# Performance work log

Hardware: AMD Instinct MI355X
Metric: run time of the kernel (lower is better)

Reference implementation:

```python
import jax, jax.numpy as jnp
import numpy as np

N_NODES = 19000   # STRING PPI nodes
N_EDGES = 600000  # avg degree ~32
B = 4096          # batch of perturbations
GNN = 256         # gnn_dim
H = 512           # hidden_dim
MID = 2048        # hidden_dim * expand
L = 6             # n_layers residual blocks
C = 3             # n_classes
R = 512           # bilinear_rank
G = 6640          # n_genes_out
LN_EPS = 1e-5


def _ln(x, scale, bias):
    mu = jnp.mean(x, axis=-1, keepdims=True)
    var = jnp.var(x, axis=-1, keepdims=True)
    return (x - mu) * jax.lax.rsqrt(var + LN_EPS) * scale + bias


def setup_inputs() -> dict:
    key = jax.random.key(0)
    ks = iter(jax.random.split(key, 24))
    s = lambda *sh: jax.random.normal(next(ks), sh, dtype=jnp.float32) * 0.02
    inp = {
        # -1 marks unknown genes (fallback embedding path)
        "node_indices": jax.random.randint(next(ks), (B,), -1, N_NODES),
        "edge_index": jax.random.randint(next(ks), (2, N_EDGES), 0, N_NODES),
        "edge_weight": jax.random.uniform(next(ks), (N_EDGES,), dtype=jnp.float32),
        # frozen mps.0-6 output cache (detached buffer in torch)
        "node_emb_cache": jax.random.normal(next(ks), (N_NODES, GNN), dtype=jnp.float32),
        # trainable graph tail (mps.7 modeled as GraphConv) + post_mp Linear
        "w_root": s(GNN, GNN),
        "w_neigh": s(GNN, GNN),
        "w_post": s(GNN, GNN),
        "b_post": jnp.zeros((GNN,), jnp.float32),
        "fallback_emb": s(GNN),
        # input_proj: LayerNorm(256) + Linear(256->512, no bias)
        "ln_in_scale": jnp.ones((GNN,), jnp.float32),
        "ln_in_bias": jnp.zeros((GNN,), jnp.float32),
        "w_in": s(H, GNN),
        # 6 residual blocks, stacked params
        "rb_ln_scale": jnp.ones((L, H), jnp.float32),
        "rb_ln_bias": jnp.zeros((L, H), jnp.float32),
        "rb_fc1": s(L, MID, H),
        "rb_fc2": s(L, H, MID),
        # bilinear head
        "w_bilinear": s(C * R, H),
        "out_gene_emb": s(G, R),
    }
    return inp


def reference(node_indices, edge_index, edge_weight, node_emb_cache,
              w_root, w_neigh, w_post, b_post, fallback_emb,
              ln_in_scale, ln_in_bias, w_in,
              rb_ln_scale, rb_ln_bias, rb_fc1, rb_fc2,
              w_bilinear, out_gene_emb):
    # --- trainable graph tail: mps.7 (GraphConv) + post_mp ---
    src, dst = edge_index[0], edge_index[1]
    msg = node_emb_cache[src] * edge_weight[:, None]          # [E, GNN]
    agg = jax.ops.segment_sum(msg, dst, num_segments=N_NODES)  # [N, GNN]
    x = jax.nn.relu(node_emb_cache @ w_root.T + agg @ w_neigh.T)
    node_emb = x @ w_post.T + b_post                           # [N, GNN]

    # --- gather perturbation embeddings with fallback for -1 ---
    known = node_indices >= 0
    safe = jnp.clip(node_indices, 0, None)
    pert = jnp.where(known[:, None], node_emb[safe], fallback_emb[None, :])  # [B, GNN]

    # --- input_proj + 6 residual blocks (dropout inactive in eval) ---
    h = _ln(pert, ln_in_scale, ln_in_bias) @ w_in.T            # [B, H]
    for i in range(L):
        y = _ln(h, rb_ln_scale[i], rb_ln_bias[i])
        y = jax.nn.gelu(y @ rb_fc1[i].T, approximate=False)    # exact erf GELU (torch default)
        h = y @ rb_fc2[i].T + h

    # --- bilinear head ---
    blin = (h @ w_bilinear.T).reshape(-1, C, R)                # [B, 3, R]
    logits = jnp.einsum('bcr,gr->bcg', blin, out_gene_emb)     # [B, 3, G]
    return logits
```

## Files before the change

### kernel.cpp

```cpp
#include <hip/hip_runtime.h>
#include <hip/hip_bf16.h>

#define N_NODES 19000
#define N_EDGES 600000
#define BATCH   4096
#define GNN_D   256
#define H_D     512
#define MID_D   2048
#define L_N     6
#define C_N     3
#define R_D     512
#define G_N     6640
#define LN_EPS  1e-5f
#define MAXDEG  128

typedef __attribute__((ext_vector_type(8))) short short8;
typedef __attribute__((ext_vector_type(4))) float f32x4;
typedef __hip_bfloat16 bf16;


__global__ void f32_to_bf16_kernel(const float* __restrict__ in, bf16* __restrict__ out, int n4) {
  int i = blockIdx.x * blockDim.x + threadIdx.x;
  if (i >= n4) return;
  float4 v = ((const float4*)in)[i];
  out[i * 4 + 0] = __float2bfloat16(v.x);
  out[i * 4 + 1] = __float2bfloat16(v.y);
  out[i * 4 + 2] = __float2bfloat16(v.z);
  out[i * 4 + 3] = __float2bfloat16(v.w);
}

__global__ void build_wrn_kernel(const float* __restrict__ w_root,
                                 const float* __restrict__ w_neigh,
                                 bf16* __restrict__ out) {
  int i4 = blockIdx.x * blockDim.x + threadIdx.x;
  if (i4 >= GNN_D * 2 * GNN_D / 4) return;
  int base = i4 * 4;
  int n = base >> 9;
  int k = base & 511;
  const float* src = (k < GNN_D) ? (w_root + (size_t)n * GNN_D + k)
                                 : (w_neigh + (size_t)n * GNN_D + (k - GNN_D));
  float4 v = *(const float4*)src;
  out[base + 0] = __float2bfloat16(v.x);
  out[base + 1] = __float2bfloat16(v.y);
  out[base + 2] = __float2bfloat16(v.z);
  out[base + 3] = __float2bfloat16(v.w);
}

__global__ void init_meta_kernel(int* __restrict__ flags, int* __restrict__ cursor,
                                 int* __restrict__ nuniq) {
  int i = blockIdx.x * blockDim.x + threadIdx.x;
  if (i < N_NODES) flags[i] = 0;
  if (i < BATCH) cursor[i] = 0;
  if (i == 0) *nuniq = 0;
}

__global__ void mark_needed_kernel(const int* __restrict__ idx, int* __restrict__ flags) {
  int i = blockIdx.x * blockDim.x + threadIdx.x;
  if (i < BATCH) {
    int id = idx[i];
    if (id >= 0) flags[id] = 1;
  }
}

__global__ void assign_slots_kernel(const int* __restrict__ flags, int* __restrict__ slot,
                                    int* __restrict__ uniq, int* __restrict__ nuniq) {
  int i = blockIdx.x * blockDim.x + threadIdx.x;
  if (i >= N_NODES) return;
  if (flags[i]) {
    int s = atomicAdd(nuniq, 1);
    slot[i] = s;
    uniq[s] = i;
  }
}

__global__ __launch_bounds__(256) void fill_edges_kernel(
    const int* __restrict__ ei, const float* __restrict__ ew,
    const int* __restrict__ flags, const int* __restrict__ slot,
    int* __restrict__ cursor, int* __restrict__ el_src, float* __restrict__ el_w) {
  int e = blockIdx.x * blockDim.x + threadIdx.x;
  if (e >= N_EDGES) return;
  int dst = ei[N_EDGES + e];
  if (!flags[dst]) return;
  int s = slot[dst];
  int p = atomicAdd(&cursor[s], 1);
  if (p < MAXDEG) {
    el_src[s * MAXDEG + p] = ei[e];
    el_w[s * MAXDEG + p] = ew[e];
  }
}

__global__ __launch_bounds__(256) void gather_nodes_kernel(
    const float* __restrict__ cache, const int* __restrict__ uniq,
    const int* __restrict__ cursor, const int* __restrict__ nuniq,
    const int* __restrict__ el_src, const float* __restrict__ el_w,
    bf16* __restrict__ compact2) {
  int s = blockIdx.x, t = threadIdx.x;
  bf16* row = compact2 + (size_t)s * (2 * GNN_D);
  if (s >= *nuniq) {
    row[t] = __float2bfloat16(0.f);
    row[GNN_D + t] = __float2bfloat16(0.f);
    return;
  }
  row[t] = __float2bfloat16(cache[(size_t)uniq[s] * GNN_D + t]);
  int deg = cursor[s];
  deg = (deg < MAXDEG) ? deg : MAXDEG;
  float acc = 0.f;
  for (int e = 0; e < deg; ++e) {
    int src = el_src[s * MAXDEG + e];
    float w = el_w[s * MAXDEG + e];
    acc += cache[(size_t)src * GNN_D + t] * w;
  }
  row[GNN_D + t] = __float2bfloat16(acc);
}

__global__ __launch_bounds__(256) void gather_ln_kernel(
    const float* __restrict__ embc, const int* __restrict__ slot,
    const float* __restrict__ fallback, const int* __restrict__ idx,
    const float* __restrict__ scale, const float* __restrict__ bias,
    bf16* __restrict__ out) {
  int b = blockIdx.x, t = threadIdx.x;
  int id = idx[b];
  float v = (id >= 0) ? embc[(size_t)slot[id] * GNN_D + t] : fallback[t];
  float s = v, q = v * v;
#pragma unroll
  for (int o = 32; o > 0; o >>= 1) { s += __shfl_down(s, o); q += __shfl_down(q, o); }
  __shared__ float ls[4], lq[4];
  int wv = t >> 6, ln = t & 63;
  if (ln == 0) { ls[wv] = s; lq[wv] = q; }
  __syncthreads();
  s = ls[0] + ls[1] + ls[2] + ls[3];
  q = lq[0] + lq[1] + lq[2] + lq[3];
  float mu = s * (1.f / GNN_D);
  float var = q * (1.f / GNN_D) - mu * mu;
  float r = rsqrtf(var + LN_EPS);
  out[(size_t)b * GNN_D + t] = __float2bfloat16((v - mu) * r * scale[t] + bias[t]);
}

__global__ __launch_bounds__(256) void ln512_kernel(
    const float* __restrict__ x, const float* __restrict__ scale,
    const float* __restrict__ bias, bf16* __restrict__ out) {
  int b = blockIdx.x, t = threadIdx.x;
  const float* xr = x + (size_t)b * H_D;
  float v0 = xr[t];
  float v1 = xr[256 + t];
  float s = v0 + v1, q = v0 * v0 + v1 * v1;
#pragma unroll
  for (int o = 32; o > 0; o >>= 1) { s += __shfl_down(s, o); q += __shfl_down(q, o); }
  __shared__ float ls[4], lq[4];
  int wv = t >> 6, ln = t & 63;
  if (ln == 0) { ls[wv] = s; lq[wv] = q; }
  __syncthreads();
  s = ls[0] + ls[1] + ls[2] + ls[3];
  q = lq[0] + lq[1] + lq[2] + lq[3];
  float mu = s * (1.f / H_D);
  float var = q * (1.f / H_D) - mu * mu;
  float r = rsqrtf(var + LN_EPS);
  bf16* orow = out + (size_t)b * H_D;
  orow[t]       = __float2bfloat16((v0 - mu) * r * scale[t]       + bias[t]);
  orow[256 + t] = __float2bfloat16((v1 - mu) * r * scale[256 + t] + bias[256 + t]);
}

__device__ inline float gelu_exact(float x) {
  return 0.5f * x * (1.f + erff(x * 0.70710678118654752f));
}


template <int NBN, int ACT, int OUT_BF16, int ADDC, int BIAS, int HBF, int SWZ>
__global__ __launch_bounds__(256) void gemm_mfma_kernel(
    const bf16* __restrict__ A, const bf16* __restrict__ W,
    const float* __restrict__ bias, const float* __restrict__ addC,
    void* __restrict__ Cout, bf16* __restrict__ out2,
    int M, int N, int K, int gx) {
  constexpr int BN = NBN * 64;
  constexpr int NF_N = NBN * 2;
  __shared__ __align__(16) bf16 sA[128 * 32];
  __shared__ __align__(16) bf16 sB[BN * 32];
  const int tid = threadIdx.x;
  const int lane = tid & 63;
  const int wid = tid >> 6;
  const int wr = wid >> 1, wc = wid & 1;

  int bidx, bidy;
  if (SWZ) {
    int nwg = gridDim.x;
    int bid = blockIdx.x;
    int q = nwg >> 3, r = nwg & 7;
    int xcd = bid & 7, orig = bid >> 3;
    int swz = (xcd < r ? xcd * (q + 1) : r * (q + 1) + (xcd - r) * q) + orig;
    bidx = swz % gx;
    bidy = swz / gx;
  } else {
    bidx = blockIdx.x;
    bidy = blockIdx.y;
  }
  const int bm = bidx * 128, bn = bidy * BN;

  f32x4 acc[4][NF_N];
#pragma unroll
  for (int m = 0; m < 4; ++m)
#pragma unroll
    for (int n = 0; n < NF_N; ++n) acc[m][n] = (f32x4){0.f, 0.f, 0.f, 0.f};

  const int rbase = lane & 15;
  const int g = lane >> 4;

  for (int k0 = 0; k0 < K; k0 += 32) {
#pragma unroll
    for (int i = 0; i < 2; ++i) {
      int li = i * 256 + tid;
      int row = li >> 2;
      int kq = (li & 3) << 3;
      int ar = bm + row; ar = (ar < M) ? ar : (M - 1);
      __builtin_amdgcn_global_load_lds(
          (const __attribute__((address_space(1))) void*)(A + (size_t)ar * K + k0 + kq),
          (__attribute__((address_space(3))) void*)(sA + li * 8), 16, 0, 0);
    }
#pragma unroll
    for (int i = 0; i < NBN; ++i) {
      int li = i * 256 + tid;
      int row = li >> 2;
      int kq = (li & 3) << 3;
      int br = bn + row; br = (br < N) ? br : (N - 1);
      __builtin_amdgcn_global_load_lds(
          (const __attribute__((address_space(1))) void*)(W + (size_t)br * K + k0 + kq),
          (__attribute__((address_space(3))) void*)(sB + li * 8), 16, 0, 0);
    }
    __syncthreads();

    short8 af[4], bfrag[NF_N];
#pragma unroll
    for (int m = 0; m < 4; ++m)
      af[m] = *(const short8*)(sA + (wr * 64 + m * 16 + rbase) * 32 + g * 8);
#pragma unroll
    for (int n = 0; n < NF_N; ++n)
      bfrag[n] = *(const short8*)(sB + (wc * (NBN * 32) + n * 16 + rbase) * 32 + g * 8);
#pragma unroll
    for (int m = 0; m < 4; ++m)
#pragma unroll
      for (int n = 0; n < NF_N; ++n)
        acc[m][n] = __builtin_amdgcn_mfma_f32_16x16x32_bf16(af[m], bfrag[n], acc[m][n], 0, 0, 0);
    __syncthreads();
  }

  const int rb = (lane >> 4) * 4;
  const int cb = lane & 15;
#pragma unroll
  for (int m = 0; m < 4; ++m) {
#pragma unroll
    for (int n = 0; n < NF_N; ++n) {
      int col = bn + wc * (NBN * 32) + n * 16 + cb;
      if (col >= N) continue;
      int row0 = bm + wr * 64 + m * 16 + rb;
#pragma unroll
      for (int r = 0; r < 4; ++r) {
        int row = row0 + r;
        if (row >= M) continue;
        float v = acc[m][n][r];
        if (BIAS) v += bias[col];
        if (ADDC) v += addC[(size_t)row * N + col];
        if (ACT == 1) v = fmaxf(v, 0.f);
        if (ACT == 2) v = gelu_exact(v);
        if (OUT_BF16)
          ((bf16*)Cout)[(size_t)row * N + col] = __float2bfloat16(v);
        else
          ((float*)Cout)[(size_t)row * N + col] = v;
        if (HBF)
          out2[(size_t)row * N + col] = __float2bfloat16(v);
      }
    }
  }
}

template <int NBN, int ACT, int OUT_BF16, int ADDC, int BIAS, int HBF>
static void launch_mfma(const bf16* A, const bf16* W, const float* bias,
                        const float* addC, void* C, bf16* out2,
                        int M, int N, int K, hipStream_t stream) {
  dim3 grid(M / 128, (N + NBN * 64 - 1) / (NBN * 64));
  gemm_mfma_kernel<NBN, ACT, OUT_BF16, ADDC, BIAS, HBF, 0>
      <<<grid, 256, 0, stream>>>(A, W, bias, addC, C, out2, M, N, K, 0);
}


#define MB (1024u * 1024u)

extern "C" void kernel_launch(void* const* d_in, const int* in_sizes, int n_in,
                              void* d_out, int out_size, void* d_ws, size_t ws_size,
                              hipStream_t stream) {
  const int*   node_indices = (const int*)d_in[0];
  const int*   edge_index   = (const int*)d_in[1];
  const float* edge_weight  = (const float*)d_in[2];
  const float* cache        = (const float*)d_in[3];
  const float* w_root       = (const float*)d_in[4];
  const float* w_neigh      = (const float*)d_in[5];
  const float* w_post       = (const float*)d_in[6];
  const float* b_post       = (const float*)d_in[7];
  const float* fallback     = (const float*)d_in[8];
  const float* ln_in_scale  = (const float*)d_in[9];
  const float* ln_in_bias   = (const float*)d_in[10];
  const float* w_in         = (const float*)d_in[11];
  const float* rb_ln_scale  = (const float*)d_in[12];
  const float* rb_ln_bias   = (const float*)d_in[13];
  const float* rb_fc1       = (const float*)d_in[14];
  const float* rb_fc2       = (const float*)d_in[15];
  const float* w_bil        = (const float*)d_in[16];
  const float* gene         = (const float*)d_in[17];
  float* out = (float*)d_out;

  char* w = (char*)d_ws;
  bf16*  compact2 = (bf16*)(w + 0 * MB);
  bf16*  tmpc     = (bf16*)(w + 4 * MB);
  float* embc     = (float*)(w + 6 * MB);
  int*   el_src   = (int*)  (w + 10 * MB);
  float* el_w     = (float*)(w + 12 * MB);
  int*   flags    = (int*)  (w + 14 * MB);
  int*   slot     = (int*)  (w + 14 * MB + 80 * 1024);
  int*   uniq     = (int*)  (w + 14 * MB + 160 * 1024);
  int*   cursor   = (int*)  (w + 14 * MB + 180 * 1024);
  int*   nuniq    = (int*)  (w + 14 * MB + 200 * 1024);
  bf16*  ymid     = (bf16*) (w + 0 * MB);
  bf16*  pertln  = (bf16*) (w + 24 * MB);
  float* h       = (float*)(w + 26 * MB);
  bf16*  yln     = (bf16*) (w + 34 * MB);
  bf16*  h_bf    = (bf16*) (w + 38 * MB);
  bf16*  blin    = (bf16*) (w + 42 * MB);
  bf16*  w_in_bf = (bf16*) (w + 55 * MB);
  bf16*  fc1_bf  = (bf16*) (w + 56 * MB);
  bf16*  fc2_bf  = (bf16*) (w + 68 * MB);
  bf16*  wbil_bf = (bf16*) (w + 80 * MB);
  bf16*  gene_bf = (bf16*) (w + 82 * MB);
  bf16*  wrn_bf  = (bf16*) (w + 90 * MB);
  bf16*  wpost_bf= (bf16*) (w + 91 * MB);

  {
    int n4;
    n4 = H_D * GNN_D / 4;
    f32_to_bf16_kernel<<<(n4 + 255) / 256, 256, 0, stream>>>(w_in, w_in_bf, n4);
    n4 = L_N * MID_D * H_D / 4;
    f32_to_bf16_kernel<<<(n4 + 255) / 256, 256, 0, stream>>>(rb_fc1, fc1_bf, n4);
    f32_to_bf16_kernel<<<(n4 + 255) / 256, 256, 0, stream>>>(rb_fc2, fc2_bf, n4);
    n4 = C_N * R_D * H_D / 4;
    f32_to_bf16_kernel<<<(n4 + 255) / 256, 256, 0, stream>>>(w_bil, wbil_bf, n4);
    n4 = G_N * R_D / 4;
    f32_to_bf16_kernel<<<(n4 + 255) / 256, 256, 0, stream>>>(gene, gene_bf, n4);
    n4 = GNN_D * GNN_D / 4;
    f32_to_bf16_kernel<<<(n4 + 255) / 256, 256, 0, stream>>>(w_post, wpost_bf, n4);
    int nw = GNN_D * 2 * GNN_D / 4;
    build_wrn_kernel<<<(nw + 255) / 256, 256, 0, stream>>>(w_root, w_neigh, wrn_bf);
  }

  init_meta_kernel<<<(N_NODES + 255) / 256, 256, 0, stream>>>(flags, cursor, nuniq);
  mark_needed_kernel<<<(BATCH + 255) / 256, 256, 0, stream>>>(node_indices, flags);
  assign_slots_kernel<<<(N_NODES + 255) / 256, 256, 0, stream>>>(flags, slot, uniq, nuniq);
  fill_edges_kernel<<<(N_EDGES + 255) / 256, 256, 0, stream>>>(
      edge_index, edge_weight, flags, slot, cursor, el_src, el_w);
  gather_nodes_kernel<<<BATCH, 256, 0, stream>>>(
      cache, uniq, cursor, nuniq, el_src, el_w, compact2);

  launch_mfma<1, 1, 1, 0, 0, 0>(compact2, wrn_bf, nullptr, nullptr, tmpc, nullptr,
                                BATCH, GNN_D, 2 * GNN_D, stream);
  launch_mfma<1, 0, 0, 0, 1, 0>(tmpc, wpost_bf, b_post, nullptr, embc, nullptr,
                                BATCH, GNN_D, GNN_D, stream);

  gather_ln_kernel<<<BATCH, 256, 0, stream>>>(embc, slot, fallback, node_indices,
                                              ln_in_scale, ln_in_bias, pertln);
  launch_mfma<1, 0, 0, 0, 0, 0>(pertln, w_in_bf, nullptr, nullptr, h, nullptr,
                                BATCH, H_D, GNN_D, stream);

  for (int i = 0; i < L_N; ++i) {
    ln512_kernel<<<BATCH, 256, 0, stream>>>(h, rb_ln_scale + (size_t)i * H_D,
                                            rb_ln_bias + (size_t)i * H_D, yln);
    launch_mfma<2, 2, 1, 0, 0, 0>(yln, fc1_bf + (size_t)i * MID_D * H_D, nullptr, nullptr,
                                  ymid, nullptr, BATCH, MID_D, H_D, stream);
    if (i < L_N - 1)
      launch_mfma<1, 0, 0, 1, 0, 0>(ymid, fc2_bf + (size_t)i * H_D * MID_D, nullptr, h,
                                    h, nullptr, BATCH, H_D, MID_D, stream);
    else
      launch_mfma<1, 0, 0, 1, 0, 1>(ymid, fc2_bf + (size_t)i * H_D * MID_D, nullptr, h,
                                    h, h_bf, BATCH, H_D, MID_D, stream);
  }

  launch_mfma<2, 0, 1, 0, 0, 0>(h_bf, wbil_bf, nullptr, nullptr, blin, nullptr,
                                BATCH, C_N * R_D, H_D, stream);
  {
    int gx = (BATCH * C_N) / 128;
    int gy = (G_N + 127) / 128;
    int nwg = gx * gy;
    gemm_mfma_kernel<2, 0, 0, 0, 0, 0, 1><<<nwg, 256, 0, stream>>>(
        blin, gene_bf, nullptr, nullptr, out, nullptr, BATCH * C_N, G_N, R_D, gx);
  }
}
```

Measured before the change: 732.1 us.

## Double-buffer LDS tiles in MFMA GEMM and parameterize M tile size

Adds a two-stage LDS ping-pong so the next K-slice is fetched via global_load_lds while MFMAs consume the current slice, removing one barrier per iteration. Makes the M tile a template parameter and uses 64-row tiles for the narrow GEMMs (GNN, input projection, fc2, bilinear projection) to raise block counts. LDS use doubles per block, which may reduce occupancy, and smaller tiles increase redundant weight loads.

```diff
diff --git a/kernel.cpp b/kernel.cpp
--- a/kernel.cpp
+++ b/kernel.cpp
@@ -165,16 +165,18 @@
 }
 
 
-template <int NBN, int ACT, int OUT_BF16, int ADDC, int BIAS, int HBF, int SWZ>
+template <int NBM, int NBN, int ACT, int OUT_BF16, int ADDC, int BIAS, int HBF, int SWZ>
 __global__ __launch_bounds__(256) void gemm_mfma_kernel(
     const bf16* __restrict__ A, const bf16* __restrict__ W,
     const float* __restrict__ bias, const float* __restrict__ addC,
     void* __restrict__ Cout, bf16* __restrict__ out2,
     int M, int N, int K, int gx) {
+  constexpr int BM = NBM * 64;
   constexpr int BN = NBN * 64;
+  constexpr int NF_M = NBM * 2;
   constexpr int NF_N = NBN * 2;
-  __shared__ __align__(16) bf16 sA[128 * 32];
-  __shared__ __align__(16) bf16 sB[BN * 32];
+  __shared__ __align__(16) bf16 sA[2][BM * 32];
+  __shared__ __align__(16) bf16 sB[2][BN * 32];
   const int tid = threadIdx.x;
   const int lane = tid & 63;
   const int wid = tid >> 6;
@@ -193,64 +195,77 @@
     bidx = blockIdx.x;
     bidy = blockIdx.y;
   }
-  const int bm = bidx * 128, bn = bidy * BN;
-
-  f32x4 acc[4][NF_N];
-#pragma unroll
-  for (int m = 0; m < 4; ++m)
+  const int bm = bidx * BM, bn = bidy * BN;
+
+  f32x4 acc[NF_M][NF_N];
+#pragma unroll
+  for (int m = 0; m < NF_M; ++m)
 #pragma unroll
     for (int n = 0; n < NF_N; ++n) acc[m][n] = (f32x4){0.f, 0.f, 0.f, 0.f};
 
   const int rbase = lane & 15;
   const int g = lane >> 4;
-
-  for (int k0 = 0; k0 < K; k0 += 32) {
-#pragma unroll
-    for (int i = 0; i < 2; ++i) {
-      int li = i * 256 + tid;
-      int row = li >> 2;
-      int kq = (li & 3) << 3;
-      int ar = bm + row; ar = (ar < M) ? ar : (M - 1);
+  const int kq = (tid & 3) << 3;
+
+  int arow[NBM], brow[NBN];
+#pragma unroll
+  for (int i = 0; i < NBM; ++i) {
+    int r0 = bm + ((i * 256 + tid) >> 2);
+    arow[i] = (r0 < M) ? r0 : (M - 1);
+  }
+#pragma unroll
+  for (int i = 0; i < NBN; ++i) {
+    int r0 = bn + ((i * 256 + tid) >> 2);
+    brow[i] = (r0 < N) ? r0 : (N - 1);
+  }
+
+  auto stage = [&](int buf, int k0) {
+#pragma unroll
+    for (int i = 0; i < NBM; ++i)
       __builtin_amdgcn_global_load_lds(
-          (const __attribute__((address_space(1))) void*)(A + (size_t)ar * K + k0 + kq),
-          (__attribute__((address_space(3))) void*)(sA + li * 8), 16, 0, 0);
-    }
-#pragma unroll
-    for (int i = 0; i < NBN; ++i) {
-      int li = i * 256 + tid;
-      int row = li >> 2;
-      int kq = (li & 3) << 3;
-      int br = bn + row; br = (br < N) ? br : (N - 1);
+          (const __attribute__((address_space(1))) void*)(A + (size_t)arow[i] * K + k0 + kq),
+          (__attribute__((address_space(3))) void*)(&sA[buf][(i * 256 + tid) * 8]), 16, 0, 0);
+#pragma unroll
+    for (int i = 0; i < NBN; ++i)
       __builtin_amdgcn_global_load_lds(
-          (const __attribute__((address_space(1))) void*)(W + (size_t)br * K + k0 + kq),
-          (__attribute__((address_space(3))) void*)(sB + li * 8), 16, 0, 0);
-    }
-    __syncthreads();
-
-    short8 af[4], bfrag[NF_N];
-#pragma unroll
-    for (int m = 0; m < 4; ++m)
-      af[m] = *(const short8*)(sA + (wr * 64 + m * 16 + rbase) * 32 + g * 8);
+          (const __attribute__((address_space(1))) void*)(W + (size_t)brow[i] * K + k0 + kq),
+          (__attribute__((address_space(3))) void*)(&sB[buf][(i * 256 + tid) * 8]), 16, 0, 0);
+  };
+
+  const int NT = K >> 5;
+  stage(0, 0);
+  __syncthreads();
+
+  int cur = 0;
+  for (int t = 0; t < NT; ++t) {
+    if (t + 1 < NT) stage(cur ^ 1, (t + 1) << 5);
+
+    short8 af[NF_M], bfrag[NF_N];
+#pragma unroll
+    for (int m = 0; m < NF_M; ++m)
+      af[m] = *(const short8*)(&sA[cur][(wr * (NBM * 32) + m * 16 + rbase) * 32 + g * 8]);
 #pragma unroll
     for (int n = 0; n < NF_N; ++n)
-      bfrag[n] = *(const short8*)(sB + (wc * (NBN * 32) + n * 16 + rbase) * 32 + g * 8);
-#pragma unroll
-    for (int m = 0; m < 4; ++m)
+      bfrag[n] = *(const short8*)(&sB[cur][(wc * (NBN * 32) + n * 16 + rbase) * 32 + g * 8]);
+#pragma unroll
+    for (int m = 0; m < NF_M; ++m)
 #pragma unroll
       for (int n = 0; n < NF_N; ++n)
         acc[m][n] = __builtin_amdgcn_mfma_f32_16x16x32_bf16(af[m], bfrag[n], acc[m][n], 0, 0, 0);
+
     __syncthreads();
+    cur ^= 1;
   }
 
   const int rb = (lane >> 4) * 4;
   const int cb = lane & 15;
 #pragma unroll
-  for (int m = 0; m < 4; ++m) {
+  for (int m = 0; m < NF_M; ++m) {
 #pragma unroll
     for (int n = 0; n < NF_N; ++n) {
       int col = bn + wc * (NBN * 32) + n * 16 + cb;
       if (col >= N) continue;
-      int row0 = bm + wr * 64 + m * 16 + rb;
+      int row0 = bm + wr * (NBM * 32) + m * 16 + rb;
 #pragma unroll
       for (int r = 0; r < 4; ++r) {
         int row = row0 + r;
@@ -271,12 +286,12 @@
   }
 }
 
-template <int NBN, int ACT, int OUT_BF16, int ADDC, int BIAS, int HBF>
+template <int NBM, int NBN, int ACT, int OUT_BF16, int ADDC, int BIAS, int HBF>
 static void launch_mfma(const bf16* A, const bf16* W, const float* bias,
                         const float* addC, void* C, bf16* out2,
                         int M, int N, int K, hipStream_t stream) {
-  dim3 grid(M / 128, (N + NBN * 64 - 1) / (NBN * 64));
-  gemm_mfma_kernel<NBN, ACT, OUT_BF16, ADDC, BIAS, HBF, 0>
+  dim3 grid(M / (NBM * 64), (N + NBN * 64 - 1) / (NBN * 64));
+  gemm_mfma_kernel<NBM, NBN, ACT, OUT_BF16, ADDC, BIAS, HBF, 0>
       <<<grid, 256, 0, stream>>>(A, W, bias, addC, C, out2, M, N, K, 0);
 }
 
@@ -356,36 +371,36 @@
   gather_nodes_kernel<<<BATCH, 256, 0, stream>>>(
       cache, uniq, cursor, nuniq, el_src, el_w, compact2);
 
-  launch_mfma<1, 1, 1, 0, 0, 0>(compact2, wrn_bf, nullptr, nullptr, tmpc, nullptr,
-                                BATCH, GNN_D, 2 * GNN_D, stream);
-  launch_mfma<1, 0, 0, 0, 1, 0>(tmpc, wpost_bf, b_post, nullptr, embc, nullptr,
-                                BATCH, GNN_D, GNN_D, stream);
+  launch_mfma<1, 1, 1, 1, 0, 0, 0>(compact2, wrn_bf, nullptr, nullptr, tmpc, nullptr,
+                                   BATCH, GNN_D, 2 * GNN_D, stream);
+  launch_mfma<1, 1, 0, 0, 0, 1, 0>(tmpc, wpost_bf, b_post, nullptr, embc, nullptr,
+                                   BATCH, GNN_D, GNN_D, stream);
 
   gather_ln_kernel<<<BATCH, 256, 0, stream>>>(embc, slot, fallback, node_indices,
                                               ln_in_scale, ln_in_bias, pertln);
-  launch_mfma<1, 0, 0, 0, 0, 0>(pertln, w_in_bf, nullptr, nullptr, h, nullptr,
-                                BATCH, H_D, GNN_D, stream);
+  launch_mfma<1, 1, 0, 0, 0, 0, 0>(pertln, w_in_bf, nullptr, nullptr, h, nullptr,
+                                   BATCH, H_D, GNN_D, stream);
 
   for (int i = 0; i < L_N; ++i) {
     ln512_kernel<<<BATCH, 256, 0, stream>>>(h, rb_ln_scale + (size_t)i * H_D,
                                             rb_ln_bias + (size_t)i * H_D, yln);
-    launch_mfma<2, 2, 1, 0, 0, 0>(yln, fc1_bf + (size_t)i * MID_D * H_D, nullptr, nullptr,
-                                  ymid, nullptr, BATCH, MID_D, H_D, stream);
+    launch_mfma<2, 2, 2, 1, 0, 0, 0>(yln, fc1_bf + (size_t)i * MID_D * H_D, nullptr, nullptr,
+                                     ymid, nullptr, BATCH, MID_D, H_D, stream);
     if (i < L_N - 1)
-      launch_mfma<1, 0, 0, 1, 0, 0>(ymid, fc2_bf + (size_t)i * H_D * MID_D, nullptr, h,
-                                    h, nullptr, BATCH, H_D, MID_D, stream);
+      launch_mfma<1, 1, 0, 0, 1, 0, 0>(ymid, fc2_bf + (size_t)i * H_D * MID_D, nullptr, h,
+                                       h, nullptr, BATCH, H_D, MID_D, stream);
     else
-      launch_mfma<1, 0, 0, 1, 0, 1>(ymid, fc2_bf + (size_t)i * H_D * MID_D, nullptr, h,
-                                    h, h_bf, BATCH, H_D, MID_D, stream);
-  }
-
-  launch_mfma<2, 0, 1, 0, 0, 0>(h_bf, wbil_bf, nullptr, nullptr, blin, nullptr,
-                                BATCH, C_N * R_D, H_D, stream);
+      launch_mfma<1, 1, 0, 0, 1, 0, 1>(ymid, fc2_bf + (size_t)i * H_D * MID_D, nullptr, h,
+                                       h, h_bf, BATCH, H_D, MID_D, stream);
+  }
+
+  launch_mfma<1, 2, 0, 1, 0, 0, 0>(h_bf, wbil_bf, nullptr, nullptr, blin, nullptr,
+                                   BATCH, C_N * R_D, H_D, stream);
   {
     int gx = (BATCH * C_N) / 128;
     int gy = (G_N + 127) / 128;
     int nwg = gx * gy;
-    gemm_mfma_kernel<2, 0, 0, 0, 0, 0, 1><<<nwg, 256, 0, stream>>>(
+    gemm_mfma_kernel<2, 2, 0, 0, 0, 0, 0, 1><<<nwg, 256, 0, stream>>>(
         blin, gene_bf, nullptr, nullptr, out, nullptr, BATCH * C_N, G_N, R_D, gx);
   }
 }
```

New measurement: 640.1 us. -12.6%, faster.

## Replace GEMM with B-panel LDS kernel streaming A fragments from global

Applied to the files above, without the earlier changes.

Rewrites the MFMA GEMM so only the 64-column weight panel is staged in padded LDS in large K chunks, while each wave loads its A fragments directly from global memory into registers with one-step software prefetch. This cuts the number of barriers and drops A-tile LDS staging, but A reads are no longer shared through LDS across waves and rely on cache instead. It also merges the seven weight-conversion launches into one segmented kernel to cut launch overhead.

```diff
diff --git a/kernel.cpp b/kernel.cpp
--- a/kernel.cpp
+++ b/kernel.cpp
@@ -18,33 +18,49 @@
 typedef __attribute__((ext_vector_type(4))) float f32x4;
 typedef __hip_bfloat16 bf16;
 
-
-__global__ void f32_to_bf16_kernel(const float* __restrict__ in, bf16* __restrict__ out, int n4) {
+#define SEG0 32768
+#define SEG1 (SEG0 + 1572864)
+#define SEG2 (SEG1 + 1572864)
+#define SEG3 (SEG2 + 196608)
+#define SEG4 (SEG3 + 849920)
+#define SEG5 (SEG4 + 16384)
+#define SEG6 (SEG5 + 32768)
+#define CONV_TOT SEG6
+
+__global__ void convert_weights_kernel(
+    const float* __restrict__ w_in, const float* __restrict__ fc1,
+    const float* __restrict__ fc2, const float* __restrict__ wbil,
+    const float* __restrict__ gene, const float* __restrict__ wpost,
+    const float* __restrict__ wroot, const float* __restrict__ wneigh,
+    bf16* __restrict__ o_win, bf16* __restrict__ o_fc1, bf16* __restrict__ o_fc2,
+    bf16* __restrict__ o_wbil, bf16* __restrict__ o_gene, bf16* __restrict__ o_wpost,
+    bf16* __restrict__ o_wrn) {
   int i = blockIdx.x * blockDim.x + threadIdx.x;
-  if (i >= n4) return;
-  float4 v = ((const float4*)in)[i];
-  out[i * 4 + 0] = __float2bfloat16(v.x);
-  out[i * 4 + 1] = __float2bfloat16(v.y);
-  out[i * 4 + 2] = __float2bfloat16(v.z);
-  out[i * 4 + 3] = __float2bfloat16(v.w);
-}
-
-__global__ void build_wrn_kernel(const float* __restrict__ w_root,
-                                 const float* __restrict__ w_neigh,
-                                 bf16* __restrict__ out) {
-  int i4 = blockIdx.x * blockDim.x + threadIdx.x;
-  if (i4 >= GNN_D * 2 * GNN_D / 4) return;
-  int base = i4 * 4;
-  int n = base >> 9;
-  int k = base & 511;
-  const float* src = (k < GNN_D) ? (w_root + (size_t)n * GNN_D + k)
-                                 : (w_neigh + (size_t)n * GNN_D + (k - GNN_D));
+  if (i >= CONV_TOT) return;
+  const float* src;
+  bf16* dst;
+  if (i < SEG0)      { src = w_in  + (size_t)i * 4;            dst = o_win  + (size_t)i * 4; }
+  else if (i < SEG1) { size_t j = i - SEG0; src = fc1  + j * 4; dst = o_fc1  + j * 4; }
+  else if (i < SEG2) { size_t j = i - SEG1; src = fc2  + j * 4; dst = o_fc2  + j * 4; }
+  else if (i < SEG3) { size_t j = i - SEG2; src = wbil + j * 4; dst = o_wbil + j * 4; }
+  else if (i < SEG4) { size_t j = i - SEG3; src = gene + j * 4; dst = o_gene + j * 4; }
+  else if (i < SEG5) { size_t j = i - SEG4; src = wpost+ j * 4; dst = o_wpost+ j * 4; }
+  else {
+    int j = i - SEG5;
+    int base = j * 4;
+    int n = base >> 9;
+    int k = base & 511;
+    src = (k < GNN_D) ? (wroot + (size_t)n * GNN_D + k)
+                      : (wneigh + (size_t)n * GNN_D + (k - GNN_D));
+    dst = o_wrn + base;
+  }
   float4 v = *(const float4*)src;
-  out[base + 0] = __float2bfloat16(v.x);
-  out[base + 1] = __float2bfloat16(v.y);
-  out[base + 2] = __float2bfloat16(v.z);
-  out[base + 3] = __float2bfloat16(v.w);
-}
+  dst[0] = __float2bfloat16(v.x);
+  dst[1] = __float2bfloat16(v.y);
+  dst[2] = __float2bfloat16(v.z);
+  dst[3] = __float2bfloat16(v.w);
+}
+
 
 __global__ void init_meta_kernel(int* __restrict__ flags, int* __restrict__ cursor,
                                  int* __restrict__ nuniq) {
@@ -165,20 +181,22 @@
 }
 
 
-template <int NBN, int ACT, int OUT_BF16, int ADDC, int BIAS, int HBF, int SWZ>
-__global__ __launch_bounds__(256) void gemm_mfma_kernel(
+template <int NWM, int NWN, int KCHUNK, int ACT, int OUT_BF16, int ADDC, int BIAS,
+          int HBF, int SWZ>
+__global__ __launch_bounds__(256) void gemm_bpanel_kernel(
     const bf16* __restrict__ A, const bf16* __restrict__ W,
     const float* __restrict__ bias, const float* __restrict__ addC,
     void* __restrict__ Cout, bf16* __restrict__ out2,
     int M, int N, int K, int gx) {
-  constexpr int BN = NBN * 64;
-  constexpr int NF_N = NBN * 2;
-  __shared__ __align__(16) bf16 sA[128 * 32];
-  __shared__ __align__(16) bf16 sB[BN * 32];
+  constexpr int BM = NWM * 64;
+  constexpr int NF_N = 4 / NWN;
+  constexpr int LDB = KCHUNK + 8;
+  __shared__ __align__(16) bf16 sB[64 * LDB];
+
   const int tid = threadIdx.x;
   const int lane = tid & 63;
   const int wid = tid >> 6;
-  const int wr = wid >> 1, wc = wid & 1;
+  const int wm = wid % NWM, wn = wid / NWM;
 
   int bidx, bidy;
   if (SWZ) {
@@ -193,53 +211,72 @@
     bidx = blockIdx.x;
     bidy = blockIdx.y;
   }
-  const int bm = bidx * 128, bn = bidy * BN;
-
-  f32x4 acc[4][NF_N];
-#pragma unroll
-  for (int m = 0; m < 4; ++m)
-#pragma unroll
-    for (int n = 0; n < NF_N; ++n) acc[m][n] = (f32x4){0.f, 0.f, 0.f, 0.f};
+  const int bm = bidx * BM, bn = bidy * 64;
 
   const int rbase = lane & 15;
   const int g = lane >> 4;
 
-  for (int k0 = 0; k0 < K; k0 += 32) {
-#pragma unroll
-    for (int i = 0; i < 2; ++i) {
-      int li = i * 256 + tid;
-      int row = li >> 2;
-      int kq = (li & 3) << 3;
-      int ar = bm + row; ar = (ar < M) ? ar : (M - 1);
-      __builtin_amdgcn_global_load_lds(
-          (const __attribute__((address_space(1))) void*)(A + (size_t)ar * K + k0 + kq),
-          (__attribute__((address_space(3))) void*)(sA + li * 8), 16, 0, 0);
-    }
-#pragma unroll
-    for (int i = 0; i < NBN; ++i) {
-      int li = i * 256 + tid;
-      int row = li >> 2;
-      int kq = (li & 3) << 3;
-      int br = bn + row; br = (br < N) ? br : (N - 1);
-      __builtin_amdgcn_global_load_lds(
-          (const __attribute__((address_space(1))) void*)(W + (size_t)br * K + k0 + kq),
-          (__attribute__((address_space(3))) void*)(sB + li * 8), 16, 0, 0);
+  const bf16* aptr[4];
+#pragma unroll
+  for (int m = 0; m < 4; ++m) {
+    int r = bm + wm * 64 + m * 16 + rbase;
+    r = (r < M) ? r : (M - 1);
+    aptr[m] = A + (size_t)r * K + g * 8;
+  }
+
+  f32x4 acc[4][NF_N];
+#pragma unroll
+  for (int m = 0; m < 4; ++m)
+#pragma unroll
+    for (int n = 0; n < NF_N; ++n) acc[m][n] = (f32x4){0.f, 0.f, 0.f, 0.f};
+
+  const int bcol = wn * (NF_N * 16);
+  const int NCH = K / KCHUNK;
+
+  for (int ch = 0; ch < NCH; ++ch) {
+    if (ch) __syncthreads();
+    constexpr int ITERS = (64 * KCHUNK) / (256 * 8);
+#pragma unroll
+    for (int it = 0; it < ITERS; ++it) {
+      int idx = it * 256 + tid;
+      int row = idx / (KCHUNK / 8);
+      int kk = (idx % (KCHUNK / 8)) * 8;
+      int br = bn + row;
+      br = (br < N) ? br : (N - 1);
+      *(short8*)(sB + row * LDB + kk) =
+          *(const short8*)(W + (size_t)br * K + (size_t)ch * KCHUNK + kk);
     }
     __syncthreads();
 
-    short8 af[4], bfrag[NF_N];
+    short8 afC[4], bfC[NF_N];
 #pragma unroll
     for (int m = 0; m < 4; ++m)
-      af[m] = *(const short8*)(sA + (wr * 64 + m * 16 + rbase) * 32 + g * 8);
+      afC[m] = *(const short8*)(aptr[m] + (size_t)ch * KCHUNK);
 #pragma unroll
     for (int n = 0; n < NF_N; ++n)
-      bfrag[n] = *(const short8*)(sB + (wc * (NBN * 32) + n * 16 + rbase) * 32 + g * 8);
-#pragma unroll
-    for (int m = 0; m < 4; ++m)
-#pragma unroll
-      for (int n = 0; n < NF_N; ++n)
-        acc[m][n] = __builtin_amdgcn_mfma_f32_16x16x32_bf16(af[m], bfrag[n], acc[m][n], 0, 0, 0);
-    __syncthreads();
+      bfC[n] = *(const short8*)(sB + (bcol + n * 16 + rbase) * LDB + g * 8);
+
+#pragma unroll 2
+    for (int kk = 0; kk < KCHUNK; kk += 32) {
+      short8 afN[4], bfN[NF_N];
+      if (kk + 32 < KCHUNK) {
+#pragma unroll
+        for (int m = 0; m < 4; ++m)
+          afN[m] = *(const short8*)(aptr[m] + (size_t)ch * KCHUNK + kk + 32);
+#pragma unroll
+        for (int n = 0; n < NF_N; ++n)
+          bfN[n] = *(const short8*)(sB + (bcol + n * 16 + rbase) * LDB + kk + 32 + g * 8);
+      }
+#pragma unroll
+      for (int m = 0; m < 4; ++m)
+#pragma unroll
+        for (int n = 0; n < NF_N; ++n)
+          acc[m][n] = __builtin_amdgcn_mfma_f32_16x16x32_bf16(afC[m], bfC[n], acc[m][n], 0, 0, 0);
+#pragma unroll
+      for (int m = 0; m < 4; ++m) afC[m] = afN[m];
+#pragma unroll
+      for (int n = 0; n < NF_N; ++n) bfC[n] = bfN[n];
+    }
   }
 
   const int rb = (lane >> 4) * 4;
@@ -248,9 +285,9 @@
   for (int m = 0; m < 4; ++m) {
 #pragma unroll
     for (int n = 0; n < NF_N; ++n) {
-      int col = bn + wc * (NBN * 32) + n * 16 + cb;
+      int col = bn + bcol + n * 16 + cb;
       if (col >= N) continue;
-      int row0 = bm + wr * 64 + m * 16 + rb;
+      int row0 = bm + wm * 64 + m * 16 + rb;
 #pragma unroll
       for (int r = 0; r < 4; ++r) {
         int row = row0 + r;
@@ -271,12 +308,12 @@
   }
 }
 
-template <int NBN, int ACT, int OUT_BF16, int ADDC, int BIAS, int HBF>
-static void launch_mfma(const bf16* A, const bf16* W, const float* bias,
-                        const float* addC, void* C, bf16* out2,
-                        int M, int N, int K, hipStream_t stream) {
-  dim3 grid(M / 128, (N + NBN * 64 - 1) / (NBN * 64));
-  gemm_mfma_kernel<NBN, ACT, OUT_BF16, ADDC, BIAS, HBF, 0>
+template <int NWM, int NWN, int KCHUNK, int ACT, int OUT_BF16, int ADDC, int BIAS, int HBF>
+static void launch_bpanel(const bf16* A, const bf16* W, const float* bias,
+                          const float* addC, void* C, bf16* out2,
+                          int M, int N, int K, hipStream_t stream) {
+  dim3 grid(M / (NWM * 64), (N + 63) / 64);
+  gemm_bpanel_kernel<NWM, NWN, KCHUNK, ACT, OUT_BF16, ADDC, BIAS, HBF, 0>
       <<<grid, 256, 0, stream>>>(A, W, bias, addC, C, out2, M, N, K, 0);
 }
 
@@ -331,22 +368,9 @@
   bf16*  wrn_bf  = (bf16*) (w + 90 * MB);
   bf16*  wpost_bf= (bf16*) (w + 91 * MB);
 
-  {
-    int n4;
-    n4 = H_D * GNN_D / 4;
-    f32_to_bf16_kernel<<<(n4 + 255) / 256, 256, 0, stream>>>(w_in, w_in_bf, n4);
-    n4 = L_N * MID_D * H_D / 4;
-    f32_to_bf16_kernel<<<(n4 + 255) / 256, 256, 0, stream>>>(rb_fc1, fc1_bf, n4);
-    f32_to_bf16_kernel<<<(n4 + 255) / 256, 256, 0, stream>>>(rb_fc2, fc2_bf, n4);
-    n4 = C_N * R_D * H_D / 4;
-    f32_to_bf16_kernel<<<(n4 + 255) / 256, 256, 0, stream>>>(w_bil, wbil_bf, n4);
-    n4 = G_N * R_D / 4;
-    f32_to_bf16_kernel<<<(n4 + 255) / 256, 256, 0, stream>>>(gene, gene_bf, n4);
-    n4 = GNN_D * GNN_D / 4;
-    f32_to_bf16_kernel<<<(n4 + 255) / 256, 256, 0, stream>>>(w_post, wpost_bf, n4);
-    int nw = GNN_D * 2 * GNN_D / 4;
-    build_wrn_kernel<<<(nw + 255) / 256, 256, 0, stream>>>(w_root, w_neigh, wrn_bf);
-  }
+  convert_weights_kernel<<<(CONV_TOT + 255) / 256, 256, 0, stream>>>(
+      w_in, rb_fc1, rb_fc2, w_bil, gene, w_post, w_root, w_neigh,
+      w_in_bf, fc1_bf, fc2_bf, wbil_bf, gene_bf, wpost_bf, wrn_bf);
 
   init_meta_kernel<<<(N_NODES + 255) / 256, 256, 0, stream>>>(flags, cursor, nuniq);
   mark_needed_kernel<<<(BATCH + 255) / 256, 256, 0, stream>>>(node_indices, flags);
@@ -356,36 +380,39 @@
   gather_nodes_kernel<<<BATCH, 256, 0, stream>>>(
       cache, uniq, cursor, nuniq, el_src, el_w, compact2);
 
-  launch_mfma<1, 1, 1, 0, 0, 0>(compact2, wrn_bf, nullptr, nullptr, tmpc, nullptr,
-                                BATCH, GNN_D, 2 * GNN_D, stream);
-  launch_mfma<1, 0, 0, 0, 1, 0>(tmpc, wpost_bf, b_post, nullptr, embc, nullptr,
-                                BATCH, GNN_D, GNN_D, stream);
+  launch_bpanel<4, 1, 512, 1, 1, 0, 0, 0>(compact2, wrn_bf, nullptr, nullptr, tmpc, nullptr,
+                                          BATCH, GNN_D, 2 * GNN_D, stream);
+  launch_bpanel<4, 1, 256, 0, 0, 0, 1, 0>(tmpc, wpost_bf, b_post, nullptr, embc, nullptr,
+                                          BATCH, GNN_D, GNN_D, stream);
 
   gather_ln_kernel<<<BATCH, 256, 0, stream>>>(embc, slot, fallback, node_indices,
                                               ln_in_scale, ln_in_bias, pertln);
-  launch_mfma<1, 0, 0, 0, 0, 0>(pertln, w_in_bf, nullptr, nullptr, h, nullptr,
-                                BATCH, H_D, GNN_D, stream);
+  launch_bpanel<4, 1, 256, 0, 0, 0, 0, 0>(pertln, w_in_bf, nullptr, nullptr, h, nullptr,
+                                          BATCH, H_D, GNN_D, stream);
 
   for (int i = 0; i < L_N; ++i) {
     ln512_kernel<<<BATCH, 256, 0, stream>>>(h, rb_ln_scale + (size_t)i * H_D,
                                             rb_ln_bias + (size_t)i * H_D, yln);
-    launch_mfma<2, 2, 1, 0, 0, 0>(yln, fc1_bf + (size_t)i * MID_D * H_D, nullptr, nullptr,
-                                  ymid, nullptr, BATCH, MID_D, H_D, stream);
+    launch_bpanel<4, 1, 512, 2, 1, 0, 0, 0>(yln, fc1_bf + (size_t)i * MID_D * H_D,
+                                            nullptr, nullptr, ymid, nullptr,
+                                            BATCH, MID_D, H_D, stream);
     if (i < L_N - 1)
-      launch_mfma<1, 0, 0, 1, 0, 0>(ymid, fc2_bf + (size_t)i * H_D * MID_D, nullptr, h,
-                                    h, nullptr, BATCH, H_D, MID_D, stream);
+      launch_bpanel<2, 2, 512, 0, 0, 1, 0, 0>(ymid, fc2_bf + (size_t)i * H_D * MID_D,
+                                              nullptr, h, h, nullptr,
+                                              BATCH, H_D, MID_D, stream);
     else
-      launch_mfma<1, 0, 0, 1, 0, 1>(ymid, fc2_bf + (size_t)i * H_D * MID_D, nullptr, h,
-                                    h, h_bf, BATCH, H_D, MID_D, stream);
-  }
-
-  launch_mfma<2, 0, 1, 0, 0, 0>(h_bf, wbil_bf, nullptr, nullptr, blin, nullptr,
-                                BATCH, C_N * R_D, H_D, stream);
+      launch_bpanel<2, 2, 512, 0, 0, 1, 0, 1>(ymid, fc2_bf + (size_t)i * H_D * MID_D,
+                                              nullptr, h, h, h_bf,
+                                              BATCH, H_D, MID_D, stream);
+  }
+
+  launch_bpanel<4, 1, 512, 0, 1, 0, 0, 0>(h_bf, wbil_bf, nullptr, nullptr, blin, nullptr,
+                                          BATCH, C_N * R_D, H_D, stream);
   {
-    int gx = (BATCH * C_N) / 128;
-    int gy = (G_N + 127) / 128;
+    int gx = (BATCH * C_N) / 256;
+    int gy = (G_N + 63) / 64;
     int nwg = gx * gy;
-    gemm_mfma_kernel<2, 0, 0, 0, 0, 0, 1><<<nwg, 256, 0, stream>>>(
+    gemm_bpanel_kernel<4, 1, 512, 0, 0, 0, 0, 0, 1><<<nwg, 256, 0, stream>>>(
         blin, gene_bf, nullptr, nullptr, out, nullptr, BATCH * C_N, G_N, R_D, gx);
   }
 }
```

Measured after the change: 862.9 us. 17.9% more time.
